# Kernel tuning notes

Measured on AMD Instinct MI355X. Metric: run time of the kernel, lower is better.

Reference implementation:

```python
import jax, jax.numpy as jnp
import numpy as np


def setup_inputs() -> dict:
    key = jax.random.key(0)
    k1, k2 = jax.random.split(key)
    group, bs, channels = 16, 16384, 128
    x = jax.random.normal(k1, (group, bs, channels), dtype=jnp.float32)
    weight = jax.random.normal(k2, (group, channels, channels), dtype=jnp.float32)
    return {"x": x, "weight": weight}


def reference(x, weight):
    """Sequential Householder reflection composition.

    x:      (group, m, n)
    weight: (group, n, channels) with channels == n; column i is the i-th reflector.
    Each step: x <- x - 2/(w^T w) * (x w) w^T  with w = weight[:, :, i].
    """
    # (channels, group, n): reflector for each scan step
    ws = jnp.moveaxis(weight, -1, 0)

    def step(xc, w):
        # w: (group, n)
        denom = jnp.sum(w * w, axis=-1)[:, None]            # (group, 1)
        xw = jnp.einsum('gmn,gn->gm', xc, w)                # (group, m)
        coef = (2.0 * xw) / denom                           # (group, m)
        xc = xc - coef[:, :, None] * w[:, None, :]          # (group, m, n)
        return xc, None

    out, _ = jax.lax.scan(step, x, ws)
    return out
```

## Files before the change

kernel.cpp:

```cpp
#include <hip/hip_runtime.h>
#include <stdint.h>

typedef __attribute__((ext_vector_type(8))) short short8;
typedef __attribute__((ext_vector_type(4))) float f32x4;
typedef unsigned short u16;

#define GROUPS 16
#define MROWS  16384
#define NCH    128

__device__ __forceinline__ u16 f2bf(float f) {
    uint32_t u = __float_as_uint(f);
    u += 0x7FFFu + ((u >> 16) & 1u);
    return (u16)(u >> 16);
}

__global__ __launch_bounds__(256) void build_q(const float* __restrict__ w,
                                               u16* __restrict__ qt) {
    __shared__ float wt[128 * 128];
    const int g   = blockIdx.y;
    const int rb  = blockIdx.x;
    const int tid = threadIdx.x;
    const float* wg = w + (size_t)g * NCH * NCH;

    const int ci = tid & 127;
    float den = 0.f;
    for (int r = 0; r < 128; r += 4) {
        float a0 = wg[(r + 0) * 128 + ci];
        float a1 = wg[(r + 1) * 128 + ci];
        float a2 = wg[(r + 2) * 128 + ci];
        float a3 = wg[(r + 3) * 128 + ci];
        den += a0 * a0 + a1 * a1 + a2 * a2 + a3 * a3;
    }
    if (tid < 128) wt[tid] = sqrtf(2.0f / den);
    __syncthreads();
    const float scl = wt[ci];
    __syncthreads();

    {
        const int h = tid >> 7;
        for (int p = 0; p < 64; ++p) {
            int r = 2 * p + h;
            wt[ci * 128 + ((r + 4 * ci) & 127)] = wg[r * 128 + ci] * scl;
        }
    }
    __syncthreads();

    const int t = rb * 16 + (tid >> 4);
    const int s = tid & 15;
    float q[8];
#pragma unroll
    for (int u = 0; u < 2; ++u)
#pragma unroll
        for (int e = 0; e < 4; ++e)
            q[u * 4 + e] = (4 * s + 64 * u + e == t) ? 1.0f : 0.0f;

    const f32x4* wt4 = (const f32x4*)wt;
    for (int i = 0; i < 128; ++i) {
        f32x4 v0 = wt4[i * 32 + ((s + 0  + i) & 31)];
        f32x4 v1 = wt4[i * 32 + ((s + 16 + i) & 31)];
        float pa = q[0] * v0.x + q[1] * v0.y + q[2] * v0.z + q[3] * v0.w;
        float pb = q[4] * v1.x + q[5] * v1.y + q[6] * v1.z + q[7] * v1.w;
        pa += pb;
        pa += __shfl_xor(pa, 1);
        pa += __shfl_xor(pa, 2);
        pa += __shfl_xor(pa, 4);
        pa += __shfl_xor(pa, 8);
        q[0] -= pa * v0.x; q[1] -= pa * v0.y; q[2] -= pa * v0.z; q[3] -= pa * v0.w;
        q[4] -= pa * v1.x; q[5] -= pa * v1.y; q[6] -= pa * v1.z; q[7] -= pa * v1.w;
    }

    u16* qg = qt + (size_t)g * NCH * NCH;
#pragma unroll
    for (int u = 0; u < 2; ++u)
#pragma unroll
        for (int e = 0; e < 4; ++e)
            qg[(4 * s + 64 * u + e) * 128 + t] = f2bf(q[u * 4 + e]);
}

__global__ __launch_bounds__(256) void apply_q(const float* __restrict__ x,
                                               const u16* __restrict__ qt,
                                               float* __restrict__ out) {
    __shared__ __align__(16) char smem[64 * 256 + 128 * 256];
    const int g   = blockIdx.y;
    const int mt  = blockIdx.x;
    const int tid = threadIdx.x;
    const float* xg = x + ((size_t)g * MROWS + (size_t)mt * 64) * NCH;

#pragma unroll
    for (int p = 0; p < 8; ++p) {
        int f   = tid + 256 * p;
        int row = f >> 5;
        int k4  = f & 31;
        f32x4 v = *(const f32x4*)(xg + row * 128 + k4 * 4);
        uint32_t lo = (uint32_t)f2bf(v.x) | ((uint32_t)f2bf(v.y) << 16);
        uint32_t hi = (uint32_t)f2bf(v.z) | ((uint32_t)f2bf(v.w) << 16);
        uint32_t off = (uint32_t)(row * 256) + (((uint32_t)(k4 * 8)) ^ ((row & 7) << 4));
        *(uint2*)(smem + off) = make_uint2(lo, hi);
    }
    const u16* qg = qt + (size_t)g * NCH * NCH;
#pragma unroll
    for (int p = 0; p < 8; ++p) {
        int f   = tid + 256 * p;
        int c   = f >> 4;
        int s16 = f & 15;
        uint4 v = *(const uint4*)((const char*)qg + c * 256 + s16 * 16);
        uint32_t off = 16384u + (uint32_t)(c * 256) + (((uint32_t)(s16 * 16)) ^ ((c & 7) << 4));
        *(uint4*)(smem + off) = v;
    }
    __syncthreads();

    const int wv = tid >> 6;
    const int l  = tid & 63;
    const int lr = l & 15;
    const int lb = l >> 4;
    const int arow = wv * 16 + lr;

    f32x4 acc[8];
#pragma unroll
    for (int nt = 0; nt < 8; ++nt) { f32x4 z = {0.f, 0.f, 0.f, 0.f}; acc[nt] = z; }

#pragma unroll
    for (int kb = 0; kb < 4; ++kb) {
        int k8 = kb * 32 + lb * 8;
        short8 a = *(const short8*)(smem + arow * 256 +
                                    (((uint32_t)(k8 * 2)) ^ ((arow & 7) << 4)));
#pragma unroll
        for (int nt = 0; nt < 8; ++nt) {
            int col = nt * 16 + lr;
            short8 b = *(const short8*)(smem + 16384 + col * 256 +
                                        (((uint32_t)(k8 * 2)) ^ ((col & 7) << 4)));
            acc[nt] = __builtin_amdgcn_mfma_f32_16x16x32_bf16(a, b, acc[nt], 0, 0, 0);
        }
    }

    float* og = out + ((size_t)g * MROWS + (size_t)mt * 64 + wv * 16) * NCH;
#pragma unroll
    for (int nt = 0; nt < 8; ++nt)
#pragma unroll
        for (int r = 0; r < 4; ++r)
            og[(lb * 4 + r) * 128 + nt * 16 + lr] = acc[nt][r];
}

extern "C" void kernel_launch(void* const* d_in, const int* in_sizes, int n_in,
                              void* d_out, int out_size, void* d_ws, size_t ws_size,
                              hipStream_t stream) {
    const float* x = (const float*)d_in[0];
    const float* w = (const float*)d_in[1];
    float* out = (float*)d_out;
    u16* qtw = (u16*)d_ws;

    build_q<<<dim3(8, GROUPS), 256, 0, stream>>>(w, qtw);
    apply_q<<<dim3(MROWS / 64, GROUPS), 256, 0, stream>>>(x, qtw, out);
}
```

Baseline: 78.93 us.

## Load x directly to registers, compute transposed MFMA, prefetch multiple row tiles per block

apply_q now loads x straight from global memory into registers in MFMA operand layout, with no LDS staging. It swaps the MFMA operands so the output comes out transposed and can be written as 16-byte vector stores. Each block handles four 64-row tiles and prefetches the next tile into registers while computing the current one. This amortizes the Q load across tiles and overlaps loads with compute, but it launches fewer blocks and uses more registers.

```diff
diff --git a/kernel.cpp b/kernel.cpp
--- a/kernel.cpp
+++ b/kernel.cpp
@@ -8,6 +8,8 @@
 #define GROUPS 16
 #define MROWS  16384
 #define NCH    128
+#define TILES  4
+#define BX     64
 
 __device__ __forceinline__ u16 f2bf(float f) {
     uint32_t u = __float_as_uint(f);
@@ -81,65 +83,79 @@
 __global__ __launch_bounds__(256) void apply_q(const float* __restrict__ x,
                                                const u16* __restrict__ qt,
                                                float* __restrict__ out) {
-    __shared__ __align__(16) char smem[64 * 256 + 128 * 256];
+    __shared__ __align__(16) u16 qs[16][128][8];
     const int g   = blockIdx.y;
-    const int mt  = blockIdx.x;
+    const int bx  = blockIdx.x;
     const int tid = threadIdx.x;
-    const float* xg = x + ((size_t)g * MROWS + (size_t)mt * 64) * NCH;
+    const int wv  = tid >> 6;
+    const int l   = tid & 63;
+    const int lr  = l & 15;
+    const int lb  = l >> 4;
 
+    const size_t rowbase = (size_t)g * MROWS + (size_t)bx * (64 * TILES);
+    const float* xlane = x   + (rowbase + wv * 16 + lr) * NCH;
+    float*       olane = out + (rowbase + wv * 16 + lr) * NCH;
+
+    f32x4 xa[8], xb[8];
 #pragma unroll
-    for (int p = 0; p < 8; ++p) {
-        int f   = tid + 256 * p;
-        int row = f >> 5;
-        int k4  = f & 31;
-        f32x4 v = *(const f32x4*)(xg + row * 128 + k4 * 4);
-        uint32_t lo = (uint32_t)f2bf(v.x) | ((uint32_t)f2bf(v.y) << 16);
-        uint32_t hi = (uint32_t)f2bf(v.z) | ((uint32_t)f2bf(v.w) << 16);
-        uint32_t off = (uint32_t)(row * 256) + (((uint32_t)(k4 * 8)) ^ ((row & 7) << 4));
-        *(uint2*)(smem + off) = make_uint2(lo, hi);
+    for (int kb = 0; kb < 4; ++kb) {
+        xa[kb * 2 + 0] = *(const f32x4*)(xlane + kb * 32 + lb * 8);
+        xa[kb * 2 + 1] = *(const f32x4*)(xlane + kb * 32 + lb * 8 + 4);
     }
+
     const u16* qg = qt + (size_t)g * NCH * NCH;
 #pragma unroll
     for (int p = 0; p < 8; ++p) {
-        int f   = tid + 256 * p;
-        int c   = f >> 4;
-        int s16 = f & 15;
-        uint4 v = *(const uint4*)((const char*)qg + c * 256 + s16 * 16);
-        uint32_t off = 16384u + (uint32_t)(c * 256) + (((uint32_t)(s16 * 16)) ^ ((c & 7) << 4));
-        *(uint4*)(smem + off) = v;
+        int f = tid + 256 * p;
+        int c = f & 127;
+        int s = f >> 7;
+        *(uint4*)(&qs[s][c][0]) = *(const uint4*)(qg + c * 128 + s * 8);
     }
     __syncthreads();
 
-    const int wv = tid >> 6;
-    const int l  = tid & 63;
-    const int lr = l & 15;
-    const int lb = l >> 4;
-    const int arow = wv * 16 + lr;
+#pragma unroll
+    for (int t = 0; t < TILES; ++t) {
+        if (t < TILES - 1) {
+#pragma unroll
+            for (int kb = 0; kb < 4; ++kb) {
+                xb[kb * 2 + 0] = *(const f32x4*)(xlane + (t + 1) * 64 * NCH + kb * 32 + lb * 8);
+                xb[kb * 2 + 1] = *(const f32x4*)(xlane + (t + 1) * 64 * NCH + kb * 32 + lb * 8 + 4);
+            }
+        }
 
-    f32x4 acc[8];
+        short8 afr[4];
 #pragma unroll
-    for (int nt = 0; nt < 8; ++nt) { f32x4 z = {0.f, 0.f, 0.f, 0.f}; acc[nt] = z; }
+        for (int kb = 0; kb < 4; ++kb) {
+            f32x4 v0 = xa[kb * 2], v1 = xa[kb * 2 + 1];
+            short8 a;
+            a[0] = (short)f2bf(v0.x); a[1] = (short)f2bf(v0.y);
+            a[2] = (short)f2bf(v0.z); a[3] = (short)f2bf(v0.w);
+            a[4] = (short)f2bf(v1.x); a[5] = (short)f2bf(v1.y);
+            a[6] = (short)f2bf(v1.z); a[7] = (short)f2bf(v1.w);
+            afr[kb] = a;
+        }
+
+        f32x4 acc[8];
+#pragma unroll
+        for (int nt = 0; nt < 8; ++nt) { f32x4 z = {0.f, 0.f, 0.f, 0.f}; acc[nt] = z; }
 
 #pragma unroll
-    for (int kb = 0; kb < 4; ++kb) {
-        int k8 = kb * 32 + lb * 8;
-        short8 a = *(const short8*)(smem + arow * 256 +
-                                    (((uint32_t)(k8 * 2)) ^ ((arow & 7) << 4)));
+        for (int kb = 0; kb < 4; ++kb) {
+            const int s = kb * 4 + lb;
 #pragma unroll
-        for (int nt = 0; nt < 8; ++nt) {
-            int col = nt * 16 + lr;
-            short8 b = *(const short8*)(smem + 16384 + col * 256 +
-                                        (((uint32_t)(k8 * 2)) ^ ((col & 7) << 4)));
-            acc[nt] = __builtin_amdgcn_mfma_f32_16x16x32_bf16(a, b, acc[nt], 0, 0, 0);
+            for (int nt = 0; nt < 8; ++nt) {
+                short8 qf = *(const short8*)(&qs[s][nt * 16 + lr][0]);
+                acc[nt] = __builtin_amdgcn_mfma_f32_16x16x32_bf16(qf, afr[kb], acc[nt], 0, 0, 0);
+            }
         }
+
+#pragma unroll
+        for (int nt = 0; nt < 8; ++nt)
+            *(f32x4*)(olane + t * 64 * NCH + nt * 16 + lb * 4) = acc[nt];
+
+#pragma unroll
+        for (int i = 0; i < 8; ++i) xa[i] = xb[i];
     }
-
-    float* og = out + ((size_t)g * MROWS + (size_t)mt * 64 + wv * 16) * NCH;
-#pragma unroll
-    for (int nt = 0; nt < 8; ++nt)
-#pragma unroll
-        for (int r = 0; r < 4; ++r)
-            og[(lb * 4 + r) * 128 + nt * 16 + lr] = acc[nt][r];
 }
 
 extern "C" void kernel_launch(void* const* d_in, const int* in_sizes, int n_in,
@@ -151,5 +167,5 @@
     u16* qtw = (u16*)d_ws;
 
     build_q<<<dim3(8, GROUPS), 256, 0, stream>>>(w, qtw);
-    apply_q<<<dim3(MROWS / 64, GROUPS), 256, 0, stream>>>(x, qtw, out);
+    apply_q<<<dim3(BX, GROUPS), 256, 0, stream>>>(x, qtw, out);
 }
```

New measurement: 92.51 us. +17.2%, slower.
